# Kernel tuning notes

Hardware: AMD Instinct MI355X
Metric: run time of the kernel (lower is better)

Reference implementation:

```python
import jax, jax.numpy as jnp
import numpy as np

EPS = 1e-3  # BatchNorm1d eps
NUM_GROUPS = 5


def _group_id(num):
    # branch by points-per-voxel: <2, ==2, ==3, 4..15, >=16
    return jnp.where(num < 2, 0,
           jnp.where(num < 3, 1,
           jnp.where(num < 4, 2,
           jnp.where(num < 16, 3, 4)))).astype(jnp.int32)


def setup_inputs() -> dict:
    key = jax.random.key(0)
    k1, k2, k3, k4, k5 = jax.random.split(key, 5)
    N, P, Cin, Cout = 40000, 32, 10, 64  # per-branch out = out_channels // 2 = 64
    inputs = jax.random.normal(k1, (N, P, Cin), dtype=jnp.float32)
    num = jax.random.randint(k2, (N,), 0, 33, dtype=jnp.int32)
    # stacked per-branch Linear weights [5, Cin, Cout] and BN affine params [5, Cout]
    W = jax.random.normal(k3, (NUM_GROUPS, Cin, Cout), dtype=jnp.float32) * 0.1
    gamma = jnp.ones((NUM_GROUPS, Cout), dtype=jnp.float32) + 0.1 * jax.random.normal(k4, (NUM_GROUPS, Cout), dtype=jnp.float32)
    beta = 0.1 * jax.random.normal(k5, (NUM_GROUPS, Cout), dtype=jnp.float32)
    return {"inputs": inputs, "num": num, "W": W, "gamma": gamma, "beta": beta}


def reference(inputs, num, W, gamma, beta):
    N, P, _ = inputs.shape
    g = _group_id(num)  # [N]
    # gather per-voxel weight and apply linear: fused gather-GEMM
    x = jnp.einsum('npi,nio->npo', inputs, W[g])  # [N, P, 64]
    # per-group BatchNorm (training-mode batch stats over each masked subset,
    # normalizing over voxels and points per channel, like BN1d on [Ni, C, P])
    ones = jnp.ones((N,), dtype=x.dtype)
    cnt = jax.ops.segment_sum(ones, g, num_segments=NUM_GROUPS) * P  # [5]
    sum_x = jax.ops.segment_sum(x.sum(axis=1), g, num_segments=NUM_GROUPS)        # [5, 64]
    sum_x2 = jax.ops.segment_sum((x * x).sum(axis=1), g, num_segments=NUM_GROUPS)  # [5, 64]
    denom = jnp.maximum(cnt, 1.0)[:, None]
    mean = sum_x / denom
    var = sum_x2 / denom - mean * mean  # biased variance, as BN uses for normalization
    scale = gamma * jax.lax.rsqrt(var + EPS)   # [5, 64]
    shift = beta - mean * scale                # [5, 64]
    x = x * scale[g][:, None, :] + shift[g][:, None, :]
    x = jax.nn.relu(x)
    x_max = jnp.max(x, axis=1, keepdims=True)  # [N, 1, 64]
    x_repeat = jnp.broadcast_to(x_max, (N, P, x.shape[2]))
    return jnp.concatenate([x, x_repeat], axis=2)  # [N, P, 128]
```

## Files before the change

### kernel.cpp

```cpp
#include <hip/hip_runtime.h>

#define P 32
#define CIN 10
#define COUT 64
#define NG 5
#define EPSV 1e-3f

__device__ __forceinline__ float4 f4zero() { return make_float4(0.f, 0.f, 0.f, 0.f); }
__device__ __forceinline__ void f4add(float4& a, const float4& b) {
    a.x += b.x; a.y += b.y; a.z += b.z; a.w += b.w;
}
__device__ __forceinline__ void f4maxi(float4& a, const float4& b) {
    a.x = fmaxf(a.x, b.x); a.y = fmaxf(a.y, b.y); a.z = fmaxf(a.z, b.z); a.w = fmaxf(a.w, b.w);
}
__device__ __forceinline__ int group_of(int nv) {
    return nv < 2 ? 0 : nv < 3 ? 1 : nv < 4 ? 2 : nv < 16 ? 3 : 4;
}

__global__ __launch_bounds__(256) void stats_kernel(
    const float* __restrict__ inputs, const int* __restrict__ num,
    const float* __restrict__ W, float* __restrict__ gsum,
    float* __restrict__ gsq, float* __restrict__ gcnt, int N)
{
    __shared__ float Ws[NG * CIN * COUT];
    __shared__ float ins[P * CIN];
    __shared__ float4 reds[64];
    __shared__ float4 redq[64];

    const int tid = threadIdx.x;
    for (int i = tid; i < NG * CIN * COUT / 4; i += 256)
        ((float4*)Ws)[i] = ((const float4*)W)[i];

    float4 as0 = f4zero(), as1 = f4zero(), as2 = f4zero(), as3 = f4zero(), as4 = f4zero();
    float4 aq0 = f4zero(), aq1 = f4zero(), aq2 = f4zero(), aq3 = f4zero(), aq4 = f4zero();
    int c0 = 0, c1 = 0, c2 = 0, c3 = 0, c4n = 0;

    const int c4 = tid & 15;
    const int pb = tid >> 4;

    __syncthreads();
    for (int v = blockIdx.x; v < N; v += gridDim.x) {
        const int g = group_of(num[v]);
        if (tid < P * CIN / 4)
            ((float4*)ins)[tid] = ((const float4*)inputs)[(size_t)v * (P * CIN / 4) + tid];
        __syncthreads();
        const float4* Wg = (const float4*)(Ws + g * CIN * COUT);
        float4 s = f4zero(), q = f4zero();
        #pragma unroll
        for (int pp = 0; pp < 2; ++pp) {
            const int p = pb + pp * 16;
            float4 acc = f4zero();
            #pragma unroll
            for (int i = 0; i < CIN; ++i) {
                const float a = ins[p * CIN + i];
                const float4 w = Wg[i * 16 + c4];
                acc.x = fmaf(a, w.x, acc.x);
                acc.y = fmaf(a, w.y, acc.y);
                acc.z = fmaf(a, w.z, acc.z);
                acc.w = fmaf(a, w.w, acc.w);
            }
            f4add(s, acc);
            q.x = fmaf(acc.x, acc.x, q.x);
            q.y = fmaf(acc.y, acc.y, q.y);
            q.z = fmaf(acc.z, acc.z, q.z);
            q.w = fmaf(acc.w, acc.w, q.w);
        }
        switch (g) {
            case 0: f4add(as0, s); f4add(aq0, q); if (!tid) c0++;  break;
            case 1: f4add(as1, s); f4add(aq1, q); if (!tid) c1++;  break;
            case 2: f4add(as2, s); f4add(aq2, q); if (!tid) c2++;  break;
            case 3: f4add(as3, s); f4add(aq3, q); if (!tid) c3++;  break;
            default: f4add(as4, s); f4add(aq4, q); if (!tid) c4n++; break;
        }
        __syncthreads();
    }

    float4 AS[NG] = {as0, as1, as2, as3, as4};
    float4 AQ[NG] = {aq0, aq1, aq2, aq3, aq4};
    const int lane = tid & 63;
    const int wv = tid >> 6;
    #pragma unroll
    for (int gi = 0; gi < NG; ++gi) {
        float4 s = AS[gi], q = AQ[gi];
        #pragma unroll
        for (int m = 16; m <= 32; m <<= 1) {
            s.x += __shfl_xor(s.x, m); s.y += __shfl_xor(s.y, m);
            s.z += __shfl_xor(s.z, m); s.w += __shfl_xor(s.w, m);
            q.x += __shfl_xor(q.x, m); q.y += __shfl_xor(q.y, m);
            q.z += __shfl_xor(q.z, m); q.w += __shfl_xor(q.w, m);
        }
        if (lane < 16) { reds[wv * 16 + lane] = s; redq[wv * 16 + lane] = q; }
        __syncthreads();
        if (tid < 16) {
            float4 S = reds[tid], Q = redq[tid];
            f4add(S, reds[16 + tid]); f4add(S, reds[32 + tid]); f4add(S, reds[48 + tid]);
            f4add(Q, redq[16 + tid]); f4add(Q, redq[32 + tid]); f4add(Q, redq[48 + tid]);
            atomicAdd(&gsum[gi * COUT + tid * 4 + 0], S.x);
            atomicAdd(&gsum[gi * COUT + tid * 4 + 1], S.y);
            atomicAdd(&gsum[gi * COUT + tid * 4 + 2], S.z);
            atomicAdd(&gsum[gi * COUT + tid * 4 + 3], S.w);
            atomicAdd(&gsq[gi * COUT + tid * 4 + 0], Q.x);
            atomicAdd(&gsq[gi * COUT + tid * 4 + 1], Q.y);
            atomicAdd(&gsq[gi * COUT + tid * 4 + 2], Q.z);
            atomicAdd(&gsq[gi * COUT + tid * 4 + 3], Q.w);
        }
        __syncthreads();
    }
    if (tid == 0) {
        const int CN[NG] = {c0, c1, c2, c3, c4n};
        #pragma unroll
        for (int gi = 0; gi < NG; ++gi)
            if (CN[gi]) atomicAdd(&gcnt[gi], (float)CN[gi]);
    }
}

__global__ __launch_bounds__(NG * COUT) void norm_kernel(
    const float* __restrict__ gsum, const float* __restrict__ gsq,
    const float* __restrict__ gcnt, const float* __restrict__ gamma,
    const float* __restrict__ beta, float* __restrict__ scale,
    float* __restrict__ shift)
{
    const int t = threadIdx.x;
    const int g = t >> 6;
    const float cnt = gcnt[g] * (float)P;
    const float denom = fmaxf(cnt, 1.f);
    const float mean = gsum[t] / denom;
    const float var = gsq[t] / denom - mean * mean;
    const float sc = gamma[t] * rsqrtf(var + EPSV);
    scale[t] = sc;
    shift[t] = fmaf(-mean, sc, beta[t]);
}

__global__ __launch_bounds__(256) void out_kernel(
    const float* __restrict__ inputs, const int* __restrict__ num,
    const float* __restrict__ W, const float* __restrict__ scale,
    const float* __restrict__ shift, float* __restrict__ out, int N)
{
    __shared__ float Ws[NG * CIN * COUT];
    __shared__ float4 scs[NG * 16];
    __shared__ float4 shs[NG * 16];
    __shared__ float ins[P * CIN];
    __shared__ float4 redm[64];

    const int tid = threadIdx.x;
    for (int i = tid; i < NG * CIN * COUT / 4; i += 256)
        ((float4*)Ws)[i] = ((const float4*)W)[i];
    if (tid < NG * 16) {
        scs[tid] = ((const float4*)scale)[tid];
        shs[tid] = ((const float4*)shift)[tid];
    }

    const int c4 = tid & 15;
    const int pb = tid >> 4;
    const int lane = tid & 63;
    const int wv = tid >> 6;

    __syncthreads();
    for (int v = blockIdx.x; v < N; v += gridDim.x) {
        const int g = group_of(num[v]);
        if (tid < P * CIN / 4)
            ((float4*)ins)[tid] = ((const float4*)inputs)[(size_t)v * (P * CIN / 4) + tid];
        __syncthreads();
        const float4* Wg = (const float4*)(Ws + g * CIN * COUT);
        const float4 sc = scs[g * 16 + c4];
        const float4 sh = shs[g * 16 + c4];
        float4 m = f4zero();
        #pragma unroll
        for (int pp = 0; pp < 2; ++pp) {
            const int p = pb + pp * 16;
            float4 acc = f4zero();
            #pragma unroll
            for (int i = 0; i < CIN; ++i) {
                const float a = ins[p * CIN + i];
                const float4 w = Wg[i * 16 + c4];
                acc.x = fmaf(a, w.x, acc.x);
                acc.y = fmaf(a, w.y, acc.y);
                acc.z = fmaf(a, w.z, acc.z);
                acc.w = fmaf(a, w.w, acc.w);
            }
            float4 y;
            y.x = fmaxf(fmaf(acc.x, sc.x, sh.x), 0.f);
            y.y = fmaxf(fmaf(acc.y, sc.y, sh.y), 0.f);
            y.z = fmaxf(fmaf(acc.z, sc.z, sh.z), 0.f);
            y.w = fmaxf(fmaf(acc.w, sc.w, sh.w), 0.f);
            ((float4*)out)[((size_t)v * P + p) * 32 + c4] = y;
            f4maxi(m, y);
        }
        #pragma unroll
        for (int msk = 16; msk <= 32; msk <<= 1) {
            m.x = fmaxf(m.x, __shfl_xor(m.x, msk));
            m.y = fmaxf(m.y, __shfl_xor(m.y, msk));
            m.z = fmaxf(m.z, __shfl_xor(m.z, msk));
            m.w = fmaxf(m.w, __shfl_xor(m.w, msk));
        }
        if (lane < 16) redm[wv * 16 + lane] = m;
        __syncthreads();
        float4 M = redm[c4];
        f4maxi(M, redm[16 + c4]);
        f4maxi(M, redm[32 + c4]);
        f4maxi(M, redm[48 + c4]);
        #pragma unroll
        for (int pp = 0; pp < 2; ++pp) {
            const int p = pb + pp * 16;
            ((float4*)out)[((size_t)v * P + p) * 32 + 16 + c4] = M;
        }
        __syncthreads();
    }
}

extern "C" void kernel_launch(void* const* d_in, const int* in_sizes, int n_in,
                              void* d_out, int out_size, void* d_ws, size_t ws_size,
                              hipStream_t stream)
{
    (void)n_in; (void)out_size; (void)ws_size;
    const float* inputs = (const float*)d_in[0];
    const int*   num    = (const int*)d_in[1];
    const float* W      = (const float*)d_in[2];
    const float* gamma  = (const float*)d_in[3];
    const float* beta   = (const float*)d_in[4];
    float* out = (float*)d_out;
    const int N = in_sizes[1];

    float* ws    = (float*)d_ws;
    float* gsum  = ws;
    float* gsq   = ws + 320;
    float* gcnt  = ws + 640;
    float* scale = ws + 656;
    float* shift = ws + 976;

    hipMemsetAsync(d_ws, 0, 648 * sizeof(float), stream);

    int gridA = N < 512 ? N : 512;
    stats_kernel<<<gridA, 256, 0, stream>>>(inputs, num, W, gsum, gsq, gcnt, N);
    norm_kernel<<<1, NG * COUT, 0, stream>>>(gsum, gsq, gcnt, gamma, beta, scale, shift);
    int gridC = (N + 7) / 8;
    if (gridC > 5000) gridC = 5000;
    if (gridC < 1) gridC = 1;
    out_kernel<<<gridC, 256, 0, stream>>>(inputs, num, W, scale, shift, out, N);
}
```

Measured before the change: 843.4 us.

## Assign one voxel per wavefront and drop block-level barriers in both kernels

Both the stats and output kernels now give each 64-lane wavefront its own voxel instead of one voxel per 256-thread block. Inputs are read straight from global memory as float2 pairs rather than staged through shared memory, and the per-voxel weights are held in registers. This removes the two __syncthreads per voxel and the shared-memory max reduction. Stats accumulate into per-wave shared slots indexed by group, and the grid sizes change. The cost is more register pressure and uncoalesced global reads of the 40-byte point rows.

Result: no change. 837.8 us (-0.7%).

```diff
diff --git a/kernel.cpp b/kernel.cpp
--- a/kernel.cpp
+++ b/kernel.cpp
@@ -6,15 +6,37 @@
 #define NG 5
 #define EPSV 1e-3f
 
-__device__ __forceinline__ float4 f4zero() { return make_float4(0.f, 0.f, 0.f, 0.f); }
-__device__ __forceinline__ void f4add(float4& a, const float4& b) {
-    a.x += b.x; a.y += b.y; a.z += b.z; a.w += b.w;
-}
-__device__ __forceinline__ void f4maxi(float4& a, const float4& b) {
-    a.x = fmaxf(a.x, b.x); a.y = fmaxf(a.y, b.y); a.z = fmaxf(a.z, b.z); a.w = fmaxf(a.w, b.w);
-}
 __device__ __forceinline__ int group_of(int nv) {
     return nv < 2 ? 0 : nv < 3 ? 1 : nv < 4 ? 2 : nv < 16 ? 3 : 4;
+}
+
+__device__ __forceinline__ float4 f4zero() { return make_float4(0.f, 0.f, 0.f, 0.f); }
+
+__device__ __forceinline__ float4 dot_row(const float* __restrict__ row,
+                                          const float4* __restrict__ w) {
+    const float2* r = (const float2*)row;
+    const float2 a0 = r[0], a1 = r[1], a2 = r[2], a3 = r[3], a4 = r[4];
+    float4 acc;
+    acc.x = a0.x * w[0].x; acc.y = a0.x * w[0].y; acc.z = a0.x * w[0].z; acc.w = a0.x * w[0].w;
+    acc.x = fmaf(a0.y, w[1].x, acc.x); acc.y = fmaf(a0.y, w[1].y, acc.y);
+    acc.z = fmaf(a0.y, w[1].z, acc.z); acc.w = fmaf(a0.y, w[1].w, acc.w);
+    acc.x = fmaf(a1.x, w[2].x, acc.x); acc.y = fmaf(a1.x, w[2].y, acc.y);
+    acc.z = fmaf(a1.x, w[2].z, acc.z); acc.w = fmaf(a1.x, w[2].w, acc.w);
+    acc.x = fmaf(a1.y, w[3].x, acc.x); acc.y = fmaf(a1.y, w[3].y, acc.y);
+    acc.z = fmaf(a1.y, w[3].z, acc.z); acc.w = fmaf(a1.y, w[3].w, acc.w);
+    acc.x = fmaf(a2.x, w[4].x, acc.x); acc.y = fmaf(a2.x, w[4].y, acc.y);
+    acc.z = fmaf(a2.x, w[4].z, acc.z); acc.w = fmaf(a2.x, w[4].w, acc.w);
+    acc.x = fmaf(a2.y, w[5].x, acc.x); acc.y = fmaf(a2.y, w[5].y, acc.y);
+    acc.z = fmaf(a2.y, w[5].z, acc.z); acc.w = fmaf(a2.y, w[5].w, acc.w);
+    acc.x = fmaf(a3.x, w[6].x, acc.x); acc.y = fmaf(a3.x, w[6].y, acc.y);
+    acc.z = fmaf(a3.x, w[6].z, acc.z); acc.w = fmaf(a3.x, w[6].w, acc.w);
+    acc.x = fmaf(a3.y, w[7].x, acc.x); acc.y = fmaf(a3.y, w[7].y, acc.y);
+    acc.z = fmaf(a3.y, w[7].z, acc.z); acc.w = fmaf(a3.y, w[7].w, acc.w);
+    acc.x = fmaf(a4.x, w[8].x, acc.x); acc.y = fmaf(a4.x, w[8].y, acc.y);
+    acc.z = fmaf(a4.x, w[8].z, acc.z); acc.w = fmaf(a4.x, w[8].w, acc.w);
+    acc.x = fmaf(a4.y, w[9].x, acc.x); acc.y = fmaf(a4.y, w[9].y, acc.y);
+    acc.z = fmaf(a4.y, w[9].z, acc.z); acc.w = fmaf(a4.y, w[9].w, acc.w);
+    return acc;
 }
 
 __global__ __launch_bounds__(256) void stats_kernel(
@@ -23,94 +45,90 @@
     float* __restrict__ gsq, float* __restrict__ gcnt, int N)
 {
     __shared__ float Ws[NG * CIN * COUT];
-    __shared__ float ins[P * CIN];
-    __shared__ float4 reds[64];
-    __shared__ float4 redq[64];
+    __shared__ float4 redS[4][NG][16];
+    __shared__ float4 redQ[4][NG][16];
+    __shared__ int   redC[4][NG];
 
     const int tid = threadIdx.x;
     for (int i = tid; i < NG * CIN * COUT / 4; i += 256)
         ((float4*)Ws)[i] = ((const float4*)W)[i];
-
-    float4 as0 = f4zero(), as1 = f4zero(), as2 = f4zero(), as3 = f4zero(), as4 = f4zero();
-    float4 aq0 = f4zero(), aq1 = f4zero(), aq2 = f4zero(), aq3 = f4zero(), aq4 = f4zero();
-    int c0 = 0, c1 = 0, c2 = 0, c3 = 0, c4n = 0;
-
-    const int c4 = tid & 15;
-    const int pb = tid >> 4;
-
+    for (int i = tid; i < 4 * NG * 16; i += 256) {
+        ((float4*)redS)[i] = f4zero();
+        ((float4*)redQ)[i] = f4zero();
+    }
+    if (tid < 4 * NG) ((int*)redC)[tid] = 0;
     __syncthreads();
-    for (int v = blockIdx.x; v < N; v += gridDim.x) {
+
+    const int lane = tid & 63, wv = tid >> 6;
+    const int c4 = lane & 15, pb = lane >> 4;
+    const int gw = blockIdx.x * 4 + wv;
+    const int stride = gridDim.x * 4;
+    int cnt0 = 0, cnt1 = 0, cnt2 = 0, cnt3 = 0, cnt4 = 0;
+
+    for (int v = gw; v < N; v += stride) {
         const int g = group_of(num[v]);
-        if (tid < P * CIN / 4)
-            ((float4*)ins)[tid] = ((const float4*)inputs)[(size_t)v * (P * CIN / 4) + tid];
-        __syncthreads();
+        const float* inrow = inputs + (size_t)v * (P * CIN);
+        float4 w[CIN];
         const float4* Wg = (const float4*)(Ws + g * CIN * COUT);
+        #pragma unroll
+        for (int i = 0; i < CIN; ++i) w[i] = Wg[i * 16 + c4];
+
         float4 s = f4zero(), q = f4zero();
         #pragma unroll
-        for (int pp = 0; pp < 2; ++pp) {
-            const int p = pb + pp * 16;
-            float4 acc = f4zero();
-            #pragma unroll
-            for (int i = 0; i < CIN; ++i) {
-                const float a = ins[p * CIN + i];
-                const float4 w = Wg[i * 16 + c4];
-                acc.x = fmaf(a, w.x, acc.x);
-                acc.y = fmaf(a, w.y, acc.y);
-                acc.z = fmaf(a, w.z, acc.z);
-                acc.w = fmaf(a, w.w, acc.w);
-            }
-            f4add(s, acc);
-            q.x = fmaf(acc.x, acc.x, q.x);
-            q.y = fmaf(acc.y, acc.y, q.y);
-            q.z = fmaf(acc.z, acc.z, q.z);
-            q.w = fmaf(acc.w, acc.w, q.w);
+        for (int k = 0; k < 8; ++k) {
+            const int p = pb + k * 4;
+            const float4 acc = dot_row(inrow + p * CIN, w);
+            s.x += acc.x; s.y += acc.y; s.z += acc.z; s.w += acc.w;
+            q.x = fmaf(acc.x, acc.x, q.x); q.y = fmaf(acc.y, acc.y, q.y);
+            q.z = fmaf(acc.z, acc.z, q.z); q.w = fmaf(acc.w, acc.w, q.w);
+        }
+        #pragma unroll
+        for (int msk = 16; msk <= 32; msk <<= 1) {
+            s.x += __shfl_xor(s.x, msk); s.y += __shfl_xor(s.y, msk);
+            s.z += __shfl_xor(s.z, msk); s.w += __shfl_xor(s.w, msk);
+            q.x += __shfl_xor(q.x, msk); q.y += __shfl_xor(q.y, msk);
+            q.z += __shfl_xor(q.z, msk); q.w += __shfl_xor(q.w, msk);
+        }
+        if (lane < 16) {
+            float4 S = redS[wv][g][c4];
+            S.x += s.x; S.y += s.y; S.z += s.z; S.w += s.w;
+            redS[wv][g][c4] = S;
+            float4 Q = redQ[wv][g][c4];
+            Q.x += q.x; Q.y += q.y; Q.z += q.z; Q.w += q.w;
+            redQ[wv][g][c4] = Q;
         }
         switch (g) {
-            case 0: f4add(as0, s); f4add(aq0, q); if (!tid) c0++;  break;
-            case 1: f4add(as1, s); f4add(aq1, q); if (!tid) c1++;  break;
-            case 2: f4add(as2, s); f4add(aq2, q); if (!tid) c2++;  break;
-            case 3: f4add(as3, s); f4add(aq3, q); if (!tid) c3++;  break;
-            default: f4add(as4, s); f4add(aq4, q); if (!tid) c4n++; break;
-        }
-        __syncthreads();
-    }
-
-    float4 AS[NG] = {as0, as1, as2, as3, as4};
-    float4 AQ[NG] = {aq0, aq1, aq2, aq3, aq4};
-    const int lane = tid & 63;
-    const int wv = tid >> 6;
-    #pragma unroll
-    for (int gi = 0; gi < NG; ++gi) {
-        float4 s = AS[gi], q = AQ[gi];
-        #pragma unroll
-        for (int m = 16; m <= 32; m <<= 1) {
-            s.x += __shfl_xor(s.x, m); s.y += __shfl_xor(s.y, m);
-            s.z += __shfl_xor(s.z, m); s.w += __shfl_xor(s.w, m);
-            q.x += __shfl_xor(q.x, m); q.y += __shfl_xor(q.y, m);
-            q.z += __shfl_xor(q.z, m); q.w += __shfl_xor(q.w, m);
-        }
-        if (lane < 16) { reds[wv * 16 + lane] = s; redq[wv * 16 + lane] = q; }
-        __syncthreads();
-        if (tid < 16) {
-            float4 S = reds[tid], Q = redq[tid];
-            f4add(S, reds[16 + tid]); f4add(S, reds[32 + tid]); f4add(S, reds[48 + tid]);
-            f4add(Q, redq[16 + tid]); f4add(Q, redq[32 + tid]); f4add(Q, redq[48 + tid]);
-            atomicAdd(&gsum[gi * COUT + tid * 4 + 0], S.x);
-            atomicAdd(&gsum[gi * COUT + tid * 4 + 1], S.y);
-            atomicAdd(&gsum[gi * COUT + tid * 4 + 2], S.z);
-            atomicAdd(&gsum[gi * COUT + tid * 4 + 3], S.w);
-            atomicAdd(&gsq[gi * COUT + tid * 4 + 0], Q.x);
-            atomicAdd(&gsq[gi * COUT + tid * 4 + 1], Q.y);
-            atomicAdd(&gsq[gi * COUT + tid * 4 + 2], Q.z);
-            atomicAdd(&gsq[gi * COUT + tid * 4 + 3], Q.w);
-        }
-        __syncthreads();
-    }
-    if (tid == 0) {
-        const int CN[NG] = {c0, c1, c2, c3, c4n};
-        #pragma unroll
-        for (int gi = 0; gi < NG; ++gi)
-            if (CN[gi]) atomicAdd(&gcnt[gi], (float)CN[gi]);
+            case 0: cnt0++; break; case 1: cnt1++; break; case 2: cnt2++; break;
+            case 3: cnt3++; break; default: cnt4++; break;
+        }
+    }
+    if (lane == 0) {
+        redC[wv][0] = cnt0; redC[wv][1] = cnt1; redC[wv][2] = cnt2;
+        redC[wv][3] = cnt3; redC[wv][4] = cnt4;
+    }
+    __syncthreads();
+
+    if (tid < NG * 16) {
+        const int g = tid >> 4, c = tid & 15;
+        float4 S = redS[0][g][c], Q = redQ[0][g][c];
+        #pragma unroll
+        for (int wvi = 1; wvi < 4; ++wvi) {
+            const float4 s2 = redS[wvi][g][c], q2 = redQ[wvi][g][c];
+            S.x += s2.x; S.y += s2.y; S.z += s2.z; S.w += s2.w;
+            Q.x += q2.x; Q.y += q2.y; Q.z += q2.z; Q.w += q2.w;
+        }
+        atomicAdd(&gsum[g * COUT + c * 4 + 0], S.x);
+        atomicAdd(&gsum[g * COUT + c * 4 + 1], S.y);
+        atomicAdd(&gsum[g * COUT + c * 4 + 2], S.z);
+        atomicAdd(&gsum[g * COUT + c * 4 + 3], S.w);
+        atomicAdd(&gsq[g * COUT + c * 4 + 0], Q.x);
+        atomicAdd(&gsq[g * COUT + c * 4 + 1], Q.y);
+        atomicAdd(&gsq[g * COUT + c * 4 + 2], Q.z);
+        atomicAdd(&gsq[g * COUT + c * 4 + 3], Q.w);
+    }
+    if (tid < NG) {
+        const int c = redC[0][tid] + redC[1][tid] + redC[2][tid] + redC[3][tid];
+        if (c) atomicAdd(&gcnt[tid], (float)c);
     }
 }
 
@@ -139,8 +157,6 @@
     __shared__ float Ws[NG * CIN * COUT];
     __shared__ float4 scs[NG * 16];
     __shared__ float4 shs[NG * 16];
-    __shared__ float ins[P * CIN];
-    __shared__ float4 redm[64];
 
     const int tid = threadIdx.x;
     for (int i = tid; i < NG * CIN * COUT / 4; i += 256)
@@ -149,42 +165,37 @@
         scs[tid] = ((const float4*)scale)[tid];
         shs[tid] = ((const float4*)shift)[tid];
     }
-
-    const int c4 = tid & 15;
-    const int pb = tid >> 4;
-    const int lane = tid & 63;
-    const int wv = tid >> 6;
-
     __syncthreads();
-    for (int v = blockIdx.x; v < N; v += gridDim.x) {
+
+    const int lane = tid & 63, wv = tid >> 6;
+    const int c4 = lane & 15, pb = lane >> 4;
+    const int gw = blockIdx.x * 4 + wv;
+    const int stride = gridDim.x * 4;
+
+    for (int v = gw; v < N; v += stride) {
         const int g = group_of(num[v]);
-        if (tid < P * CIN / 4)
-            ((float4*)ins)[tid] = ((const float4*)inputs)[(size_t)v * (P * CIN / 4) + tid];
-        __syncthreads();
+        const float* inrow = inputs + (size_t)v * (P * CIN);
+        float4 w[CIN];
         const float4* Wg = (const float4*)(Ws + g * CIN * COUT);
+        #pragma unroll
+        for (int i = 0; i < CIN; ++i) w[i] = Wg[i * 16 + c4];
         const float4 sc = scs[g * 16 + c4];
         const float4 sh = shs[g * 16 + c4];
+        float4* outv = (float4*)out + (size_t)v * (P * 2 * COUT / 4);
+
         float4 m = f4zero();
         #pragma unroll
-        for (int pp = 0; pp < 2; ++pp) {
-            const int p = pb + pp * 16;
-            float4 acc = f4zero();
-            #pragma unroll
-            for (int i = 0; i < CIN; ++i) {
-                const float a = ins[p * CIN + i];
-                const float4 w = Wg[i * 16 + c4];
-                acc.x = fmaf(a, w.x, acc.x);
-                acc.y = fmaf(a, w.y, acc.y);
-                acc.z = fmaf(a, w.z, acc.z);
-                acc.w = fmaf(a, w.w, acc.w);
-            }
+        for (int k = 0; k < 8; ++k) {
+            const int p = pb + k * 4;
+            const float4 acc = dot_row(inrow + p * CIN, w);
             float4 y;
             y.x = fmaxf(fmaf(acc.x, sc.x, sh.x), 0.f);
             y.y = fmaxf(fmaf(acc.y, sc.y, sh.y), 0.f);
             y.z = fmaxf(fmaf(acc.z, sc.z, sh.z), 0.f);
             y.w = fmaxf(fmaf(acc.w, sc.w, sh.w), 0.f);
-            ((float4*)out)[((size_t)v * P + p) * 32 + c4] = y;
-            f4maxi(m, y);
+            outv[p * 32 + c4] = y;
+            m.x = fmaxf(m.x, y.x); m.y = fmaxf(m.y, y.y);
+            m.z = fmaxf(m.z, y.z); m.w = fmaxf(m.w, y.w);
         }
         #pragma unroll
         for (int msk = 16; msk <= 32; msk <<= 1) {
@@ -193,18 +204,11 @@
             m.z = fmaxf(m.z, __shfl_xor(m.z, msk));
             m.w = fmaxf(m.w, __shfl_xor(m.w, msk));
         }
-        if (lane < 16) redm[wv * 16 + lane] = m;
-        __syncthreads();
-        float4 M = redm[c4];
-        f4maxi(M, redm[16 + c4]);
-        f4maxi(M, redm[32 + c4]);
-        f4maxi(M, redm[48 + c4]);
-        #pragma unroll
-        for (int pp = 0; pp < 2; ++pp) {
-            const int p = pb + pp * 16;
-            ((float4*)out)[((size_t)v * P + p) * 32 + 16 + c4] = M;
-        }
-        __syncthreads();
+        #pragma unroll
+        for (int k = 0; k < 8; ++k) {
+            const int p = pb + k * 4;
+            outv[p * 32 + 16 + c4] = m;
+        }
     }
 }
 
@@ -230,11 +234,11 @@
 
     hipMemsetAsync(d_ws, 0, 648 * sizeof(float), stream);
 
-    int gridA = N < 512 ? N : 512;
+    int gridA = (N + 3) / 4;
+    if (gridA > 1024) gridA = 1024;
     stats_kernel<<<gridA, 256, 0, stream>>>(inputs, num, W, gsum, gsq, gcnt, N);
     norm_kernel<<<1, NG * COUT, 0, stream>>>(gsum, gsq, gcnt, gamma, beta, scale, shift);
-    int gridC = (N + 7) / 8;
-    if (gridC > 5000) gridC = 5000;
-    if (gridC < 1) gridC = 1;
+    int gridC = (N + 3) / 4;
+    if (gridC > 2048) gridC = 2048;
     out_kernel<<<gridC, 256, 0, stream>>>(inputs, num, W, scale, shift, out, N);
 }
```
